# Kernel tuning notes

Hardware: AMD Instinct MI355X
Metric: run time of the kernel (lower is better)

The kernel has to match this reference:

```python
import jax, jax.numpy as jnp
import numpy as np

OBS_LEN, PRED_LEN, N, P = 8, 12, 4096, 32
EH, DH, EMB, BOT, NZ = 64, 128, 64, 1024, 8


def setup_inputs() -> dict:
    key = jax.random.key(0)
    ks = iter(jax.random.split(key, 64))
    rn = lambda shp, s=0.05: (jax.random.normal(next(ks), shp, jnp.float32) * s)
    d = {
        'obs_traj': rn((OBS_LEN, N, 2), 1.0),
        'obs_traj_rel': rn((OBS_LEN, N, 2), 0.5),
        'obs_speed': jax.random.uniform(next(ks), (OBS_LEN, N, 1), jnp.float32),
        'noise': rn((N, NZ), 1.0),
        'enc_emb_W': rn((2, EMB)), 'enc_emb_b': jnp.zeros((EMB,), jnp.float32),
        'enc_Wih': rn((EMB, 4 * EH)), 'enc_Whh': rn((EH, 4 * EH)), 'enc_b': jnp.zeros((4 * EH,), jnp.float32),
        'pool_sp_W': rn((2, 64)), 'pool_sp_b': jnp.zeros((64,), jnp.float32),
        'pool_spd_W': rn((1, 64)), 'pool_spd_b': jnp.zeros((64,), jnp.float32),
        'pool_l1_W': rn((192, 512)), 'pool_l1_b': jnp.zeros((512,), jnp.float32),
        'pool_bn1_g': jnp.ones((512,), jnp.float32), 'pool_bn1_b': jnp.zeros((512,), jnp.float32),
        'pool_l2_W': rn((512, BOT)), 'pool_l2_b': jnp.zeros((BOT,), jnp.float32),
        'pool_bn2_g': jnp.ones((BOT,), jnp.float32), 'pool_bn2_b': jnp.zeros((BOT,), jnp.float32),
        'spd_emb_W': rn((OBS_LEN, 64)), 'spd_emb_b': jnp.zeros((64,), jnp.float32),
        'ctx_l1_W': rn((EH + BOT + 64, 1024)), 'ctx_l1_b': jnp.zeros((1024,), jnp.float32),
        'ctx_bn1_g': jnp.ones((1024,), jnp.float32), 'ctx_bn1_b': jnp.zeros((1024,), jnp.float32),
        'ctx_l2_W': rn((1024, DH - NZ)), 'ctx_l2_b': jnp.zeros((DH - NZ,), jnp.float32),
        'ctx_bn2_g': jnp.ones((DH - NZ,), jnp.float32), 'ctx_bn2_b': jnp.zeros((DH - NZ,), jnp.float32),
        'dec_emb_W': rn((3, EMB)), 'dec_emb_b': jnp.zeros((EMB,), jnp.float32),
        'dec_Wih': rn((EMB, 4 * DH)), 'dec_Whh': rn((DH, 4 * DH)), 'dec_b': jnp.zeros((4 * DH,), jnp.float32),
        'h2p_W': rn((DH, 2)), 'h2p_b': jnp.zeros((2,), jnp.float32),
        'group_size': P,
    }
    return d


def _lstm(xs, Wih, Whh, b, h0, c0):
    # xs: [T, B, in]; PyTorch gate order (i, f, g, o)
    def step(carry, x):
        h, c = carry
        g = x @ Wih + h @ Whh + b
        i, f, gg, o = jnp.split(g, 4, axis=-1)
        c = jax.nn.sigmoid(f) * c + jax.nn.sigmoid(i) * jnp.tanh(gg)
        h = jax.nn.sigmoid(o) * jnp.tanh(c)
        return (h, c), h
    (h, c), _ = jax.lax.scan(step, (h0, c0), xs)
    return h, c


def _bn(x, g, b):
    # BatchNorm1d, eval mode with running_mean=0, running_var=1
    return x * g + b


def reference(obs_traj, obs_traj_rel, obs_speed, noise,
              enc_emb_W, enc_emb_b, enc_Wih, enc_Whh, enc_b,
              pool_sp_W, pool_sp_b, pool_spd_W, pool_spd_b,
              pool_l1_W, pool_l1_b, pool_bn1_g, pool_bn1_b,
              pool_l2_W, pool_l2_b, pool_bn2_g, pool_bn2_b,
              spd_emb_W, spd_emb_b,
              ctx_l1_W, ctx_l1_b, ctx_bn1_g, ctx_bn1_b,
              ctx_l2_W, ctx_l2_b, ctx_bn2_g, ctx_bn2_b,
              dec_emb_W, dec_emb_b, dec_Wih, dec_Whh, dec_b,
              h2p_W, h2p_b, group_size):
    n = obs_traj.shape[1]
    G = n // group_size
    # ---- Encoder: embed rel traj, run LSTM, take final hidden ----
    emb = obs_traj_rel @ enc_emb_W + enc_emb_b                       # [T, N, 64]
    h0 = jnp.zeros((n, EH), emb.dtype)
    final_h, _ = _lstm(emb, enc_Wih, enc_Whh, enc_b, h0, h0)         # [N, 64]
    # ---- PoolHiddenNet (vectorized per-group P x P social pooling) ----
    end_pos = obs_traj[-1].reshape(G, group_size, 2)                 # [G, P, 2]
    end_spd = obs_speed[-1].reshape(G, group_size, 1)                # [G, P, 1]
    hG = final_h.reshape(G, group_size, EH)                          # [G, P, 64]
    # rel[g, i, j] = pos[g, j] - pos[g, i]
    rel = end_pos[:, None, :, :] - end_pos[:, :, None, :]            # [G, P, P, 2]
    rel_e = rel @ pool_sp_W + pool_sp_b                              # [G, P, P, 64]
    spd_e = end_spd @ pool_spd_W + pool_spd_b                        # [G, P, 64]
    Pn = group_size
    feat = jnp.concatenate([
        rel_e,
        jnp.broadcast_to(hG[:, None, :, :], (G, Pn, Pn, EH)),
        jnp.broadcast_to(spd_e[:, None, :, :], (G, Pn, Pn, 64)),
    ], axis=-1)                                                      # [G, P, P, 192]
    h1 = jax.nn.relu(_bn(feat @ pool_l1_W + pool_l1_b, pool_bn1_g, pool_bn1_b))
    h2 = jax.nn.relu(_bn(h1 @ pool_l2_W + pool_l2_b, pool_bn2_g, pool_bn2_b))
    pool_h = jnp.max(h2, axis=2).reshape(n, BOT)                     # max over j -> [N, 1024]
    # ---- speed context: sigmoid(Linear(8 -> 64)) over obs speed history ----
    spd_hist = jnp.transpose(obs_speed[:, :, 0])                     # [N, 8]
    speed_ctx = jax.nn.sigmoid(spd_hist @ spd_emb_W + spd_emb_b)     # [N, 64]
    # ---- mlp_decoder_context + ped-level noise ----
    ctx_in = jnp.concatenate([final_h, pool_h, speed_ctx], axis=1)   # [N, 1152]
    c1 = jax.nn.relu(_bn(ctx_in @ ctx_l1_W + ctx_l1_b, ctx_bn1_g, ctx_bn1_b))
    ctx = jax.nn.relu(_bn(c1 @ ctx_l2_W + ctx_l2_b, ctx_bn2_g, ctx_bn2_b))  # [N, 120]
    dec_h = jnp.concatenate([ctx, noise], axis=1)                    # [N, 128]
    dec_c = jnp.zeros_like(dec_h)
    # ---- Decoder rollout (pred_len steps) ----
    last_pos = obs_traj[-1]
    last_speed = obs_speed[-1]                                       # [N, 1]
    x0 = jnp.concatenate([obs_traj_rel[-1], last_speed], axis=1) @ dec_emb_W + dec_emb_b

    def step(carry, _):
        h, c, x, lp = carry
        g = x @ dec_Wih + h @ dec_Whh + dec_b
        i, f, gg, o = jnp.split(g, 4, axis=-1)
        c = jax.nn.sigmoid(f) * c + jax.nn.sigmoid(i) * jnp.tanh(gg)
        h = jax.nn.sigmoid(o) * jnp.tanh(c)
        rel_pos = h @ h2p_W + h2p_b                                  # [N, 2]
        cur = rel_pos + lp
        x = jnp.concatenate([rel_pos, last_speed], axis=1) @ dec_emb_W + dec_emb_b
        return (h, c, x, cur), rel_pos

    _, rels = jax.lax.scan(step, (dec_h, dec_c, x0, last_pos), None, length=PRED_LEN)
    return rels  # [pred_len, N, 2]
```

## Files before the change

kernel.cpp:

```cpp
#include <hip/hip_runtime.h>

typedef __attribute__((ext_vector_type(8))) short v8s;
typedef __attribute__((ext_vector_type(4))) float v4f;
typedef unsigned short u16;

#define DINL static __device__ __forceinline__

DINL float b2f(u16 u){ union { unsigned uu; float ff; } x; x.uu = ((unsigned)u)<<16; return x.ff; }
DINL u16 f2b(float f){ union { float ff; unsigned uu; } x; x.ff = f; unsigned r = x.uu + 0x7FFFu + ((x.uu>>16)&1u); return (u16)(r>>16); }
DINL u16 f2b_hu(float f){ union { float ff; unsigned uu; } x; x.ff = f; return (u16)((x.uu + 0x8000u)>>16); }
DINL float sigm(float x){ return 1.0f/(1.0f+__expf(-x)); }
DINL float tanh_(float x){ return 2.0f/(1.0f+__expf(-2.0f*x)) - 1.0f; }
DINL float ld(const void* p, int i, int isf){
    return isf ? ((const float*)p)[i] : b2f(((const u16*)p)[i]);
}
DINL void g2lds16(const u16* g, u16* l){
    __builtin_amdgcn_global_load_lds(
        (const __attribute__((address_space(1))) unsigned int*)g,
        (__attribute__((address_space(3))) unsigned int*)l, 16, 0, 0);
}
DINL int detect_isf(const void* obs_speed){
    const u16* p = (const u16*)obs_speed;
    int f = 0;
    for (int i = 0; i < 16; ++i){
        u16 v = p[2*i];
        if ((v & 0x8000u) || v > 0x3F80u) f = 1;
    }
    return f;
}

#define FLAG_OFF 0x000000
#define AUX_OFF  0x000100
#define ENCF_OFF 0x010000
#define DECF_OFF 0x020000
#define CW2T_OFF 0x050000
#define W2T_OFF  0x090000
#define DECH_OFF 0x090000
#define CW1T_OFF 0x190000
#define IT_OFF   0x3D0000
#define IR_OFF   0x3F0000
#define IS_OFF   0x410000
#define INZ_OFF  0x420000
#define IW1H_OFF 0x430000
#define SM_OFF   0x440000
#define CTX_OFF  0x450000
#define AV_OFF   0xD50000
#define BIG_NEED 0x1550000

#define SM_EEW 0
#define SM_EEB 128
#define SM_ENB 192
#define SM_DEW 448
#define SM_DEB 640
#define SM_DNB 704
#define SM_H2W 1216
#define SM_H2B 1472
#define SM_SEW 1536
#define SM_SEB 2048

DINL void trans_tile(const void* in, u16* out, int K, int N, int isf,
                     int bx, int by, int t, float tile[64][65])
{
    const int nbase = bx*64, kbase = by*64;
    const int c = t & 63, r0 = (t >> 6)*16;
    for (int rep = 0; rep < 16; ++rep){
        int r = r0 + rep;
        int n = nbase + c;
        float v = 0.f;
        if (n < N) v = ld(in, (kbase + r)*N + n, isf);
        tile[r][c] = v;
    }
    __syncthreads();
    for (int rep = 0; rep < 16; ++rep){
        int r = r0 + rep;
        out[(size_t)(nbase + r)*K + kbase + c] = f2b(tile[c][r]);
    }
}

__global__ __launch_bounds__(256) void k_prep(
    const void* obs_traj, const void* obs_rel, const void* obs_speed, const void* noise,
    const void* eeW, const void* eeB, const void* enc_Wih, const void* enc_Whh, const void* encB,
    const void* spW, const void* spB, const void* spdW, const void* spdB,
    const void* pool_l1_W, const void* l1B, const void* bn1g, const void* bn1b,
    const void* pool_l2_W, const void* l2b, const void* bn2g, const void* bn2b,
    const void* seW, const void* seB,
    const void* ctx_l1_W, const void* c1b, const void* cbn1g, const void* cbn1b,
    const void* ctx_l2_W, const void* c2b, const void* cbn2g, const void* cbn2b,
    const void* deW, const void* deB, const void* dec_Wih, const void* dec_Whh, const void* decB,
    const void* h2W, const void* h2B,
    int* flag, float* AUX,
    u16* IT, u16* IR, u16* IS, u16* INZ, u16* IW1H, u16* SM,
    u16* W2T, u16* cW1T, u16* cW2T, u16* encF, u16* decF)
{
    __shared__ float tile[64][65];
    __shared__ int sisf;
    const int t = threadIdx.x;
    if (t == 0){
        int f = detect_isf(obs_speed);
        sisf = f;
        if (blockIdx.x == 0) *flag = f;
    }
    __syncthreads();
    const int isf = sisf;
    int bid = blockIdx.x;
    if (bid < 905){
        int idx = bid*256 + t;
        if (idx < 65536){ IT[idx] = f2b(ld(obs_traj, idx, isf)); return; }
        idx -= 65536;
        if (idx < 65536){ IR[idx] = f2b(ld(obs_rel, idx, isf)); return; }
        idx -= 65536;
        if (idx < 32768){ IS[idx] = f2b(ld(obs_speed, idx, isf)); return; }
        idx -= 32768;
        if (idx < 32768){ INZ[idx] = f2b(ld(noise, idx, isf)); return; }
        idx -= 32768;
        if (idx < 32768){ IW1H[idx] = f2b(ld(pool_l1_W, idx + 32768, isf)); return; }
        idx -= 32768;
        if (idx < 128){ SM[SM_EEW + idx] = f2b(ld(eeW, idx, isf)); return; }
        idx -= 128;
        if (idx < 64){ SM[SM_EEB + idx] = f2b(ld(eeB, idx, isf)); return; }
        idx -= 64;
        if (idx < 256){ SM[SM_ENB + idx] = f2b(ld(encB, idx, isf)); return; }
        idx -= 256;
        if (idx < 192){ SM[SM_DEW + idx] = f2b(ld(deW, idx, isf)); return; }
        idx -= 192;
        if (idx < 64){ SM[SM_DEB + idx] = f2b(ld(deB, idx, isf)); return; }
        idx -= 64;
        if (idx < 512){ SM[SM_DNB + idx] = f2b(ld(decB, idx, isf)); return; }
        idx -= 512;
        if (idx < 256){ SM[SM_H2W + idx] = f2b(ld(h2W, idx, isf)); return; }
        idx -= 256;
        if (idx < 2){ SM[SM_H2B + idx] = f2b(ld(h2B, idx, isf)); return; }
        idx -= 2;
        if (idx < 512){ SM[SM_SEW + idx] = f2b(ld(seW, idx, isf)); return; }
        idx -= 512;
        if (idx < 64){ SM[SM_SEB + idx] = f2b(ld(seB, idx, isf)); return; }
        return;
    }
    bid -= 905;
    if (bid < 512){
        int idx = bid*256 + t;
        if (idx < 32768){
            int jj = idx&7, lane = (idx>>3)&63, kcnf = idx>>9;
            int kc = kcnf&3, nf = kcnf>>2;
            int k = kc*32 + (lane>>4)*8 + jj, n = nf*16 + (lane&15);
            encF[idx] = (k < 64) ? f2b(ld(enc_Wih, k*256+n, isf)) : f2b(ld(enc_Whh, (k-64)*256+n, isf));
        } else {
            idx -= 32768;
            int jj = idx&7, lane = (idx>>3)&63, kcnf = idx>>9;
            int kc = kcnf % 6, nf = kcnf / 6;
            int k = kc*32 + (lane>>4)*8 + jj, n = nf*16 + (lane&15);
            decF[idx] = (k < 64) ? f2b(ld(dec_Wih, k*512+n, isf)) : f2b(ld(dec_Whh, (k-64)*512+n, isf));
        }
        return;
    }
    bid -= 512;
    if (bid < 128){ trans_tile(pool_l2_W, W2T, 512, 1024, isf, bid & 15, bid >> 4, t, tile); return; }
    bid -= 128;
    if (bid < 288){ trans_tile(ctx_l1_W, cW1T, 1152, 1024, isf, bid & 15, bid >> 4, t, tile); return; }
    bid -= 288;
    if (bid < 32){ trans_tile(ctx_l2_W, cW2T, 1024, 120, isf, bid & 1, bid >> 1, t, tile); return; }
    bid -= 32;
    {
        int idx = bid*256 + t;
        if (idx < 512){
            int c = idx;
            float m0 = 0.f, m1 = 0.f, qv = 0.f, cv = 0.f;
            for (int e = 0; e < 64; ++e){
                float w1a = ld(pool_l1_W, e*512 + c, isf);
                m0 += ld(spW, e, isf)*w1a;
                m1 += ld(spW, 64+e, isf)*w1a;
                cv += ld(spB, e, isf)*w1a;
                float w1c = ld(pool_l1_W, (128+e)*512 + c, isf);
                qv += ld(spdW, e, isf)*w1c;
                cv += ld(spdB, e, isf)*w1c;
            }
            cv += ld(l1B, c, isf);
            float g1 = ld(bn1g, c, isf), bb1 = ld(bn1b, c, isf);
            AUX[c] = m0; AUX[512+c] = m1; AUX[1024+c] = qv; AUX[1536+c] = cv;
            AUX[2048+c] = g1; AUX[2560+c] = bb1;
            AUX[3072+c] = g1*m0; AUX[3584+c] = g1*m1;
            return;
        }
        idx -= 512;
        if (idx < 1024){
            float g = ld(bn2g, idx, isf);
            AUX[4096+idx] = g; AUX[5120+idx] = ld(l2b, idx, isf)*g + ld(bn2b, idx, isf);
            return;
        }
        idx -= 1024;
        if (idx < 1024){
            float g = ld(cbn1g, idx, isf);
            AUX[6144+idx] = g; AUX[7168+idx] = ld(c1b, idx, isf)*g + ld(cbn1b, idx, isf);
            return;
        }
        idx -= 1024;
        if (idx < 128){
            int c = idx;
            float g  = (c < 120) ? ld(cbn2g, c, isf) : 1.f;
            float bb = (c < 120) ? (ld(c2b, c, isf)*g + ld(cbn2b, c, isf)) : 0.f;
            AUX[8192+c] = g; AUX[8320+c] = bb;
        }
    }
}

__global__ __launch_bounds__(256) void k_encoder(
    const u16* __restrict__ rel, const u16* __restrict__ embW, const u16* __restrict__ embB,
    const u16* __restrict__ encF, const u16* __restrict__ encB,
    const u16* __restrict__ IT, const u16* __restrict__ IS, const u16* __restrict__ IW1H,
    const u16* __restrict__ sW, const u16* __restrict__ sB,
    const float* __restrict__ AUX,
    u16* __restrict__ ctxIn, u16* __restrict__ Avec)
{
    __shared__ __align__(16) u16 Als[16*136];
    __shared__ float pxs[16], pys[16], sps[16];
    const int t = threadIdx.x, pedbase = blockIdx.x*16;
    const int w = t>>6, lane = t&63, quad = lane>>4, l15 = lane&15;
    for (int idx = t; idx < 16*64; idx += 256){ int p = idx>>6, jj = idx&63; Als[p*136 + 64 + jj] = 0; }
    if (t < 16){
        pxs[t] = b2f(IT[7*8192 + (pedbase+t)*2 + 0]);
        pys[t] = b2f(IT[7*8192 + (pedbase+t)*2 + 1]);
        sps[t] = b2f(IS[7*4096 + pedbase + t]);
    }
    {
        int p = t>>4, e0 = (t&15)*4;
        float rx = b2f(rel[(pedbase+p)*2 + 0]);
        float ry = b2f(rel[(pedbase+p)*2 + 1]);
        for (int e = e0; e < e0+4; ++e)
            Als[p*136 + e] = f2b(rx*b2f(embW[e]) + ry*b2f(embW[64+e]) + b2f(embB[e]));
    }
    const int j = w*16 + l15;
    const float bi = b2f(encB[j]), bff = b2f(encB[64+j]), bg = b2f(encB[128+j]), bo = b2f(encB[192+j]);
    float c4[4] = {0.f,0.f,0.f,0.f};
    for (int step = 0; step < 8; ++step){
        __syncthreads();
        v4f acc[4];
        for (int q = 0; q < 4; ++q) acc[q] = (v4f){0.f,0.f,0.f,0.f};
        for (int kc = 0; kc < 4; ++kc){
            v8s a = *(const v8s*)&Als[l15*136 + kc*32 + quad*8];
            for (int q = 0; q < 4; ++q){
                int nf = q*4 + w;
                v8s b = *(const v8s*)&encF[((nf*4 + kc)*64 + lane)*8];
                acc[q] = __builtin_amdgcn_mfma_f32_16x16x32_bf16(a, b, acc[q], 0, 0, 0);
            }
        }
        __syncthreads();
        for (int r = 0; r < 4; ++r){
            float gi = sigm(acc[0][r] + bi), gf = sigm(acc[1][r] + bff);
            float gg = tanh_(acc[2][r] + bg), go = sigm(acc[3][r] + bo);
            c4[r] = gf*c4[r] + gi*gg;
            Als[(quad*4 + r)*136 + 64 + j] = f2b(go*tanh_(c4[r]));
        }
        if (step < 7){
            int p = t>>4, e0 = (t&15)*4;
            float rx = b2f(rel[(step+1)*8192 + (pedbase+p)*2 + 0]);
            float ry = b2f(rel[(step+1)*8192 + (pedbase+p)*2 + 1]);
            for (int e = e0; e < e0+4; ++e)
                Als[p*136 + e] = f2b(rx*b2f(embW[e]) + ry*b2f(embW[64+e]) + b2f(embB[e]));
        }
    }
    __syncthreads();
    for (int idx = t; idx < 1024; idx += 256){
        int p = idx>>6, e = idx&63;
        ctxIn[(size_t)(pedbase+p)*1152 + e] = Als[p*136 + 64 + e];
    }
    {
        const int c0 = (t&127)*4, pg = (t>>7)*8;
        float4 acc[8];
        for (int p = 0; p < 8; ++p) acc[p] = make_float4(0.f,0.f,0.f,0.f);
        for (int e = 0; e < 64; ++e){
            ushort4 wv = *(const ushort4*)(IW1H + e*512 + c0);
            float w0 = b2f(wv.x), w1 = b2f(wv.y), w2 = b2f(wv.z), w3 = b2f(wv.w);
            for (int p = 0; p < 8; ++p){
                float h = b2f(Als[(pg+p)*136 + 64 + e]);
                acc[p].x += h*w0; acc[p].y += h*w1; acc[p].z += h*w2; acc[p].w += h*w3;
            }
        }
        float4 m0 = *(const float4*)(AUX + c0),        m1 = *(const float4*)(AUX + 512 + c0);
        float4 qv = *(const float4*)(AUX + 1024 + c0), cv = *(const float4*)(AUX + 1536 + c0);
        float4 g1 = *(const float4*)(AUX + 2048 + c0), bb = *(const float4*)(AUX + 2560 + c0);
        for (int p = 0; p < 8; ++p){
            float px = pxs[pg+p], py = pys[pg+p], sp = sps[pg+p];
            ushort4 o;
            o.x = f2b(g1.x*(px*m0.x + py*m1.x + sp*qv.x + cv.x + acc[p].x) + bb.x);
            o.y = f2b(g1.y*(px*m0.y + py*m1.y + sp*qv.y + cv.y + acc[p].y) + bb.y);
            o.z = f2b(g1.z*(px*m0.z + py*m1.z + sp*qv.z + cv.z + acc[p].z) + bb.z);
            o.w = f2b(g1.w*(px*m0.w + py*m1.w + sp*qv.w + cv.w + acc[p].w) + bb.w);
            *(ushort4*)&Avec[(size_t)(pedbase+pg+p)*512 + c0] = o;
        }
    }
    {
        int s = t & 63;
        for (int rep = 0; rep < 4; ++rep){
            int p = (t>>6)*4 + rep;
            int nid = pedbase + p;
            float a = b2f(sB[s]);
            for (int tt = 0; tt < 8; ++tt) a += b2f(IS[tt*4096 + nid]) * b2f(sW[tt*64 + s]);
            ctxIn[(size_t)nid*1152 + 1088 + s] = f2b(sigm(a));
        }
    }
}

__global__ __launch_bounds__(256, 3) void k_pool(
    const u16* __restrict__ Avec, const u16* __restrict__ W2T,
    const u16* __restrict__ IT, const float* __restrict__ AUX,
    u16* __restrict__ ctxIn)
{
    __shared__ __align__(16) u16 Als[64*72];
    __shared__ __align__(16) u16 Bls[256*64];
    __shared__ __align__(16) float pmls[1024];
    const int t = threadIdx.x;
    const int g = blockIdx.x >> 4, ip = blockIdx.x & 15;
    const int n0 = blockIdx.y * 256;
    const int w = t>>6, lane = t&63, quad = lane>>4, l15 = lane&15;
    const int aj = t>>3, ao = t&7;
    const float px0 = b2f(IT[7*8192 + (g*32 + ip*2 + 0)*2 + 0]);
    const float py0 = b2f(IT[7*8192 + (g*32 + ip*2 + 0)*2 + 1]);
    const float px1 = b2f(IT[7*8192 + (g*32 + ip*2 + 1)*2 + 0]);
    const float py1 = b2f(IT[7*8192 + (g*32 + ip*2 + 1)*2 + 1]);
    for (int i = t; i < 512; i += 256){
        float m0 = AUX[3072 + i], m1 = AUX[3584 + i];
        pmls[i]       = px0*m0 + py0*m1;
        pmls[512 + i] = px1*m0 + py1*m1;
    }
    const u16* bsrc = W2T + (size_t)(n0 + w*8 + (lane>>3))*512 + (size_t)(((lane&7) ^ (lane>>3)))*8;
    u16* bdst = &Bls[w*512];
    const u16* arow = Avec + (size_t)(g*32+aj)*512 + ao*8;
    v4f acc[4][4];
    for (int mf = 0; mf < 4; ++mf) for (int nf = 0; nf < 4; ++nf) acc[mf][nf] = (v4f){0.f,0.f,0.f,0.f};
    union { v8s v; u16 u[8]; } av;
    av.v = *(const v8s*)arow;
    for (int ch = 0; ch < 8; ++ch){
        const int k0 = ch*64;
        __syncthreads();
        for (int it = 0; it < 8; ++it)
            g2lds16(bsrc + k0 + it*16384, bdst + it*2048);
        {
            float a0[8];
            #pragma unroll
            for (int i = 0; i < 8; ++i) a0[i] = b2f(av.u[i]);
            #pragma unroll
            for (int il = 0; il < 2; ++il){
                float4 p0 = *(const float4*)&pmls[il*512 + k0 + ao*8];
                float4 p1 = *(const float4*)&pmls[il*512 + k0 + ao*8 + 4];
                float pmv[8] = {p0.x,p0.y,p0.z,p0.w,p1.x,p1.y,p1.z,p1.w};
                union { unsigned u[4]; v8s v; } pk;
                #pragma unroll
                for (int jj = 0; jj < 4; ++jj){
                    union { float f; unsigned u; } x0, x1;
                    x0.f = fmaxf(a0[2*jj]   - pmv[2*jj],   0.f);
                    x1.f = fmaxf(a0[2*jj+1] - pmv[2*jj+1], 0.f);
                    pk.u[jj] = __builtin_amdgcn_perm(x1.u + 0x8000u, x0.u + 0x8000u, 0x07060302u);
                }
                *(v8s*)&Als[(il*32+aj)*72 + ao*8] = pk.v;
            }
        }
        if (ch < 7) av.v = *(const v8s*)(arow + (ch+1)*64);
        __syncthreads();
        for (int kc = 0; kc < 2; ++kc){
            v8s af[4];
            for (int mf = 0; mf < 4; ++mf)
                af[mf] = *(const v8s*)&Als[(mf*16 + l15)*72 + kc*32 + quad*8];
            const int sl = ((kc*4 + quad) ^ (l15&7))*8;
            #pragma unroll
            for (int nf = 0; nf < 4; ++nf){
                v8s bf = *(const v8s*)&Bls[(w*64 + nf*16 + l15)*64 + sl];
                acc[0][nf] = __builtin_amdgcn_mfma_f32_16x16x32_bf16(af[0], bf, acc[0][nf], 0, 0, 0);
                acc[1][nf] = __builtin_amdgcn_mfma_f32_16x16x32_bf16(af[1], bf, acc[1][nf], 0, 0, 0);
                acc[2][nf] = __builtin_amdgcn_mfma_f32_16x16x32_bf16(af[2], bf, acc[2][nf], 0, 0, 0);
                acc[3][nf] = __builtin_amdgcn_mfma_f32_16x16x32_bf16(af[3], bf, acc[3][nf], 0, 0, 0);
            }
        }
    }
    const float* S2 = AUX + 4096; const float* B2 = AUX + 5120;
    for (int nf = 0; nf < 4; ++nf){
        int n = n0 + w*64 + nf*16 + l15;
        float s = S2[n], bb = B2[n];
        float mm0 = 0.f, mm1 = 0.f;
        for (int mf = 0; mf < 2; ++mf) for (int r = 0; r < 4; ++r) mm0 = fmaxf(mm0, fmaxf(s*acc[mf][nf][r] + bb, 0.f));
        for (int mf = 2; mf < 4; ++mf) for (int r = 0; r < 4; ++r) mm1 = fmaxf(mm1, fmaxf(s*acc[mf][nf][r] + bb, 0.f));
        mm0 = fmaxf(mm0, __shfl_xor(mm0, 16)); mm0 = fmaxf(mm0, __shfl_xor(mm0, 32));
        mm1 = fmaxf(mm1, __shfl_xor(mm1, 16)); mm1 = fmaxf(mm1, __shfl_xor(mm1, 32));
        if (quad == 0) ctxIn[(size_t)(g*32 + ip*2 + 0)*1152 + 64 + n] = f2b(mm0);
        if (quad == 1) ctxIn[(size_t)(g*32 + ip*2 + 1)*1152 + 64 + n] = f2b(mm1);
    }
}

template<int MF>
__global__ __launch_bounds__(256) void k_gemm_bt(
    const u16* __restrict__ A, int lda, const u16* __restrict__ BT,
    const float* __restrict__ S, const float* __restrict__ Bb,
    u16* __restrict__ out, int ldo, int K, int validN,
    const u16* __restrict__ noisep)
{
    __shared__ __align__(16) u16 Als[MF*32*72];
    __shared__ __align__(16) u16 Bls[128*72];
    const int t = threadIdx.x;
    const int m0 = blockIdx.x*(MF*32), n0 = blockIdx.y*128;
    const int w = t>>6, lane = t&63, quad = lane>>4, l15 = lane&15;
    const int rw = w>>1, cw = w&1;
    v4f acc[MF][4];
    for (int mf = 0; mf < MF; ++mf) for (int nf = 0; nf < 4; ++nf) acc[mf][nf] = (v4f){0.f,0.f,0.f,0.f};
    const int nch = K >> 6;
    for (int ch = 0; ch < nch; ++ch){
        const int k0 = ch*64;
        __syncthreads();
        if (MF == 4){
            const int srow = t>>1, sh = t&1;
            const u16* srcA = A + (size_t)(m0+srow)*lda + k0 + sh*32;
            u16* dstA = &Als[srow*72 + sh*32];
            ((v8s*)dstA)[0] = ((const v8s*)srcA)[0];
            ((v8s*)dstA)[1] = ((const v8s*)srcA)[1];
            ((v8s*)dstA)[2] = ((const v8s*)srcA)[2];
            ((v8s*)dstA)[3] = ((const v8s*)srcA)[3];
        } else {
            const int srow = t>>2, sh = t&3;
            const u16* srcA = A + (size_t)(m0+srow)*lda + k0 + sh*16;
            u16* dstA = &Als[srow*72 + sh*16];
            ((v8s*)dstA)[0] = ((const v8s*)srcA)[0];
            ((v8s*)dstA)[1] = ((const v8s*)srcA)[1];
        }
        {
            const int srow = t>>1, sh = t&1;
            const u16* srcB = BT + (size_t)(n0+srow)*K + k0 + sh*32;
            u16* dstB = &Bls[srow*72 + sh*32];
            ((v8s*)dstB)[0] = ((const v8s*)srcB)[0];
            ((v8s*)dstB)[1] = ((const v8s*)srcB)[1];
            ((v8s*)dstB)[2] = ((const v8s*)srcB)[2];
            ((v8s*)dstB)[3] = ((const v8s*)srcB)[3];
        }
        __syncthreads();
        for (int kc = 0; kc < 2; ++kc){
            v8s af[MF], bf[4];
            for (int mf = 0; mf < MF; ++mf) af[mf] = *(const v8s*)&Als[(rw*(MF*16) + mf*16 + l15)*72 + kc*32 + quad*8];
            for (int nf = 0; nf < 4; ++nf) bf[nf] = *(const v8s*)&Bls[(cw*64 + nf*16 + l15)*72 + kc*32 + quad*8];
            for (int mf = 0; mf < MF; ++mf)
                for (int nf = 0; nf < 4; ++nf)
                    acc[mf][nf] = __builtin_amdgcn_mfma_f32_16x16x32_bf16(af[mf], bf[nf], acc[mf][nf], 0, 0, 0);
        }
    }
    for (int nf = 0; nf < 4; ++nf){
        int n = n0 + cw*64 + nf*16 + l15;
        bool okn = (n < validN);
        float s = okn ? S[n] : 0.f, bb = okn ? Bb[n] : 0.f;
        bool okz = (!okn) && (noisep != nullptr) && (n < 128);
        for (int mf = 0; mf < MF; ++mf){
            int m = m0 + rw*(MF*16) + mf*16 + quad*4;
            for (int r = 0; r < 4; ++r){
                float v = fmaxf(s*acc[mf][nf][r] + bb, 0.f);
                if (okn) out[(size_t)(m+r)*ldo + n] = f2b(v);
                else if (okz) out[(size_t)(m+r)*ldo + n] = noisep[(size_t)(m+r)*8 + (n - 120)];
            }
        }
    }
}

__global__ __launch_bounds__(256) void k_decoder(
    const u16* __restrict__ decH0, const u16* __restrict__ decF, const u16* __restrict__ decB,
    const u16* __restrict__ dembW, const u16* __restrict__ dembB,
    const u16* __restrict__ h2pW, const u16* __restrict__ h2pB,
    const u16* __restrict__ obs_rel, const u16* __restrict__ obs_speed,
    const int* __restrict__ flag, void* __restrict__ outp)
{
    __shared__ __align__(16) u16 Als[16*200];
    __shared__ float rps[16][2];
    __shared__ float sps[16];
    __shared__ float h2ps[256];
    const int t = threadIdx.x, pedbase = blockIdx.x*16;
    const int w = t>>6, lane = t&63, quad = lane>>4, l15 = lane&15;
    const int isf = *flag;
    for (int idx = t; idx < 2048; idx += 256){
        int p = idx>>7, jj = idx&127;
        Als[p*200 + 64 + jj] = decH0[(pedbase+p)*128 + jj];
    }
    h2ps[t] = b2f(h2pW[t]);
    if (t < 16) sps[t] = b2f(obs_speed[7*4096 + pedbase + t]);
    if (t < 32){ int p = t>>1, cmp = t&1; rps[p][cmp] = b2f(obs_rel[7*8192 + (pedbase+p)*2 + cmp]); }
    __syncthreads();
    {
        int p = t>>4, e0 = (t&15)*4;
        for (int e = e0; e < e0+4; ++e){
            float v = rps[p][0]*b2f(dembW[e]) + rps[p][1]*b2f(dembW[64+e]) + sps[p]*b2f(dembW[128+e]) + b2f(dembB[e]);
            Als[p*200 + e] = f2b(v);
        }
    }
    float bI[2], bF[2], bG[2], bO[2];
    for (int nfl = 0; nfl < 2; ++nfl){
        int j = w*32 + nfl*16 + l15;
        bI[nfl] = b2f(decB[j]); bF[nfl] = b2f(decB[128+j]);
        bG[nfl] = b2f(decB[256+j]); bO[nfl] = b2f(decB[384+j]);
    }
    float c8[2][4] = {{0.f,0.f,0.f,0.f},{0.f,0.f,0.f,0.f}};
    for (int s = 0; s < 12; ++s){
        __syncthreads();
        v4f acc[4][2];
        for (int q = 0; q < 4; ++q) for (int nfl = 0; nfl < 2; ++nfl) acc[q][nfl] = (v4f){0.f,0.f,0.f,0.f};
        for (int kc = 0; kc < 6; ++kc){
            v8s a = *(const v8s*)&Als[l15*200 + kc*32 + quad*8];
            for (int q = 0; q < 4; ++q){
                for (int nfl = 0; nfl < 2; ++nfl){
                    int nf = q*8 + w*2 + nfl;
                    v8s b = *(const v8s*)&decF[((nf*6 + kc)*64 + lane)*8];
                    acc[q][nfl] = __builtin_amdgcn_mfma_f32_16x16x32_bf16(a, b, acc[q][nfl], 0, 0, 0);
                }
            }
        }
        __syncthreads();
        for (int nfl = 0; nfl < 2; ++nfl){
            int j = w*32 + nfl*16 + l15;
            for (int r = 0; r < 4; ++r){
                float gi = sigm(acc[0][nfl][r] + bI[nfl]), gf = sigm(acc[1][nfl][r] + bF[nfl]);
                float gg = tanh_(acc[2][nfl][r] + bG[nfl]), go = sigm(acc[3][nfl][r] + bO[nfl]);
                c8[nfl][r] = gf*c8[nfl][r] + gi*gg;
                Als[(quad*4 + r)*200 + 64 + j] = f2b(go*tanh_(c8[nfl][r]));
            }
        }
        __syncthreads();
        {
            int p = t>>4, cmp = (t>>3)&1, part = t&7;
            float rp = 0.f;
            int j0 = part*16;
            for (int jj = j0; jj < j0+16; ++jj)
                rp += b2f(Als[p*200 + 64 + jj]) * h2ps[jj*2 + cmp];
            rp += __shfl_xor(rp, 1);
            rp += __shfl_xor(rp, 2);
            rp += __shfl_xor(rp, 4);
            if (part == 0){
                rp += b2f(h2pB[cmp]);
                int oi = s*8192 + (pedbase+p)*2 + cmp;
                if (isf) ((float*)outp)[oi] = rp;
                else     ((u16*)outp)[oi]   = f2b(rp);
                rps[p][cmp] = rp;
            }
        }
        __syncthreads();
        {
            int p = t>>4, e0 = (t&15)*4;
            for (int e = e0; e < e0+4; ++e){
                float v = rps[p][0]*b2f(dembW[e]) + rps[p][1]*b2f(dembW[64+e]) + sps[p]*b2f(dembW[128+e]) + b2f(dembB[e]);
                Als[p*200 + e] = f2b(v);
            }
        }
    }
}

extern "C" void kernel_launch(void* const* d_in, const int* in_sizes, int n_in,
                              void* d_out, int out_size, void* d_ws, size_t ws_size,
                              hipStream_t stream)
{
    (void)in_sizes; (void)n_in; (void)out_size;
    const void* obs_traj  = d_in[0];
    const void* obs_rel   = d_in[1];
    const void* obs_speed = d_in[2];
    const void* noise     = d_in[3];
    const void* enc_emb_W = d_in[4];
    const void* enc_emb_b = d_in[5];
    const void* enc_Wih   = d_in[6];
    const void* enc_Whh   = d_in[7];
    const void* enc_b     = d_in[8];
    const void* pool_sp_W = d_in[9];
    const void* pool_sp_b = d_in[10];
    const void* pool_spd_W= d_in[11];
    const void* pool_spd_b= d_in[12];
    const void* pool_l1_W = d_in[13];
    const void* pool_l1_b = d_in[14];
    const void* pool_bn1_g= d_in[15];
    const void* pool_bn1_b= d_in[16];
    const void* pool_l2_W = d_in[17];
    const void* pool_l2_b = d_in[18];
    const void* pool_bn2_g= d_in[19];
    const void* pool_bn2_b= d_in[20];
    const void* spd_emb_W = d_in[21];
    const void* spd_emb_b = d_in[22];
    const void* ctx_l1_W  = d_in[23];
    const void* ctx_l1_b  = d_in[24];
    const void* ctx_bn1_g = d_in[25];
    const void* ctx_bn1_b = d_in[26];
    const void* ctx_l2_W  = d_in[27];
    const void* ctx_l2_b  = d_in[28];
    const void* ctx_bn2_g = d_in[29];
    const void* ctx_bn2_b = d_in[30];
    const void* dec_emb_W = d_in[31];
    const void* dec_emb_b = d_in[32];
    const void* dec_Wih   = d_in[33];
    const void* dec_Whh   = d_in[34];
    const void* dec_b     = d_in[35];
    const void* h2p_W     = d_in[36];
    const void* h2p_b     = d_in[37];

    char* ws = (char*)d_ws;
    int*   flag  = (int*)  (ws + FLAG_OFF);
    float* AUX   = (float*)(ws + AUX_OFF);
    u16*   encF  = (u16*)  (ws + ENCF_OFF);
    u16*   decF  = (u16*)  (ws + DECF_OFF);
    u16*   cW2T  = (u16*)  (ws + CW2T_OFF);
    u16*   W2T   = (u16*)  (ws + W2T_OFF);
    u16*   decH  = (u16*)  (ws + DECH_OFF);
    u16*   cW1T  = (u16*)  (ws + CW1T_OFF);
    u16*   IT    = (u16*)  (ws + IT_OFF);
    u16*   IR    = (u16*)  (ws + IR_OFF);
    u16*   IS    = (u16*)  (ws + IS_OFF);
    u16*   INZ   = (u16*)  (ws + INZ_OFF);
    u16*   IW1H  = (u16*)  (ws + IW1H_OFF);
    u16*   SM    = (u16*)  (ws + SM_OFF);
    u16*   ctxIn = (u16*)  (ws + CTX_OFF);
    u16*   Avec  = (u16*)  (ws + AV_OFF);
    u16*   c1    = (u16*)  (ws + AV_OFF);
    const bool big = (ws_size >= (size_t)BIG_NEED);

    k_prep<<<dim3(1876), dim3(256), 0, stream>>>(
        obs_traj, obs_rel, obs_speed, noise,
        enc_emb_W, enc_emb_b, enc_Wih, enc_Whh, enc_b,
        pool_sp_W, pool_sp_b, pool_spd_W, pool_spd_b,
        pool_l1_W, pool_l1_b, pool_bn1_g, pool_bn1_b,
        pool_l2_W, pool_l2_b, pool_bn2_g, pool_bn2_b,
        spd_emb_W, spd_emb_b,
        ctx_l1_W, ctx_l1_b, ctx_bn1_g, ctx_bn1_b,
        ctx_l2_W, ctx_l2_b, ctx_bn2_g, ctx_bn2_b,
        dec_emb_W, dec_emb_b, dec_Wih, dec_Whh, dec_b,
        h2p_W, h2p_b,
        flag, AUX, IT, IR, IS, INZ, IW1H, SM,
        W2T, cW1T, cW2T, encF, decF);
    k_encoder<<<dim3(256), dim3(256), 0, stream>>>(
        IR, SM + SM_EEW, SM + SM_EEB, encF, SM + SM_ENB,
        IT, IS, IW1H, SM + SM_SEW, SM + SM_SEB, AUX, ctxIn, Avec);
    k_pool<<<dim3(2048, 4), dim3(256), 0, stream>>>(Avec, W2T, IT, AUX, ctxIn);
    if (big){
        k_gemm_bt<4><<<dim3(32, 8), dim3(256), 0, stream>>>(
            ctxIn, 1152, cW1T, AUX + 6144, AUX + 7168, c1, 1024, 1152, 1024, (const u16*)nullptr);
        k_gemm_bt<2><<<dim3(64, 1), dim3(256), 0, stream>>>(
            c1, 1024, cW2T, AUX + 8192, AUX + 8320, decH, 128, 1024, 120, INZ);
    } else {
        k_gemm_bt<4><<<dim3(16, 8), dim3(256), 0, stream>>>(
            ctxIn, 1152, cW1T, AUX + 6144, AUX + 7168, c1, 1024, 1152, 1024, (const u16*)nullptr);
        k_gemm_bt<2><<<dim3(32, 1), dim3(256), 0, stream>>>(
            c1, 1024, cW2T, AUX + 8192, AUX + 8320, decH, 128, 1024, 120, INZ);
        k_gemm_bt<4><<<dim3(16, 8), dim3(256), 0, stream>>>(
            ctxIn + (size_t)2048*1152, 1152, cW1T, AUX + 6144, AUX + 7168, c1, 1024, 1152, 1024, (const u16*)nullptr);
        k_gemm_bt<2><<<dim3(32, 1), dim3(256), 0, stream>>>(
            c1, 1024, cW2T, AUX + 8192, AUX + 8320, decH + (size_t)2048*128, 128, 1024, 120, INZ + (size_t)2048*8);
    }
    k_decoder<<<dim3(256), dim3(256), 0, stream>>>(
        decH, decF, SM + SM_DNB, SM + SM_DEW, SM + SM_DEB,
        SM + SM_H2W, SM + SM_H2B, IR, IS, flag, d_out);
}
```

Measured before the change: 435.9 us.

## Shrink context GEMM tiles, split pool launch, shuffle decoder positions

Switches the context-MLP GEMMs to smaller M tiles (MF=2 and a new MF=1 path) with more blocks, so more CUs have work on the small problem. Splits the pool kernel into two launches of half the grid each through an x-offset parameter. In the decoder, the predicted relative positions are broadcast with wave shuffles instead of going through shared memory, which removes one barrier per step and skips the unused embedding on the final step. Smaller tiles reload the B operand more often, and the extra launch adds launch overhead.

```diff
diff --git a/kernel.cpp b/kernel.cpp
--- a/kernel.cpp
+++ b/kernel.cpp
@@ -8,7 +8,6 @@
 
 DINL float b2f(u16 u){ union { unsigned uu; float ff; } x; x.uu = ((unsigned)u)<<16; return x.ff; }
 DINL u16 f2b(float f){ union { float ff; unsigned uu; } x; x.ff = f; unsigned r = x.uu + 0x7FFFu + ((x.uu>>16)&1u); return (u16)(r>>16); }
-DINL u16 f2b_hu(float f){ union { float ff; unsigned uu; } x; x.ff = f; return (u16)((x.uu + 0x8000u)>>16); }
 DINL float sigm(float x){ return 1.0f/(1.0f+__expf(-x)); }
 DINL float tanh_(float x){ return 2.0f/(1.0f+__expf(-2.0f*x)) - 1.0f; }
 DINL float ld(const void* p, int i, int isf){
@@ -303,13 +302,14 @@
 __global__ __launch_bounds__(256, 3) void k_pool(
     const u16* __restrict__ Avec, const u16* __restrict__ W2T,
     const u16* __restrict__ IT, const float* __restrict__ AUX,
-    u16* __restrict__ ctxIn)
+    u16* __restrict__ ctxIn, int xbase)
 {
     __shared__ __align__(16) u16 Als[64*72];
     __shared__ __align__(16) u16 Bls[256*64];
     __shared__ __align__(16) float pmls[1024];
     const int t = threadIdx.x;
-    const int g = blockIdx.x >> 4, ip = blockIdx.x & 15;
+    const int bx = blockIdx.x + xbase;
+    const int g = bx >> 4, ip = bx & 15;
     const int n0 = blockIdx.y * 256;
     const int w = t>>6, lane = t&63, quad = lane>>4, l15 = lane&15;
     const int aj = t>>3, ao = t&7;
@@ -412,12 +412,17 @@
             ((v8s*)dstA)[1] = ((const v8s*)srcA)[1];
             ((v8s*)dstA)[2] = ((const v8s*)srcA)[2];
             ((v8s*)dstA)[3] = ((const v8s*)srcA)[3];
-        } else {
+        } else if (MF == 2){
             const int srow = t>>2, sh = t&3;
             const u16* srcA = A + (size_t)(m0+srow)*lda + k0 + sh*16;
             u16* dstA = &Als[srow*72 + sh*16];
             ((v8s*)dstA)[0] = ((const v8s*)srcA)[0];
             ((v8s*)dstA)[1] = ((const v8s*)srcA)[1];
+        } else {
+            const int srow = t>>3, sh = t&7;
+            const u16* srcA = A + (size_t)(m0+srow)*lda + k0 + sh*8;
+            u16* dstA = &Als[srow*72 + sh*8];
+            ((v8s*)dstA)[0] = ((const v8s*)srcA)[0];
         }
         {
             const int srow = t>>1, sh = t&1;
@@ -462,7 +467,6 @@
     const int* __restrict__ flag, void* __restrict__ outp)
 {
     __shared__ __align__(16) u16 Als[16*200];
-    __shared__ float rps[16][2];
     __shared__ float sps[16];
     __shared__ float h2ps[256];
     const int t = threadIdx.x, pedbase = blockIdx.x*16;
@@ -474,12 +478,13 @@
     }
     h2ps[t] = b2f(h2pW[t]);
     if (t < 16) sps[t] = b2f(obs_speed[7*4096 + pedbase + t]);
-    if (t < 32){ int p = t>>1, cmp = t&1; rps[p][cmp] = b2f(obs_rel[7*8192 + (pedbase+p)*2 + cmp]); }
     __syncthreads();
     {
         int p = t>>4, e0 = (t&15)*4;
+        float rx = b2f(obs_rel[7*8192 + (pedbase+p)*2 + 0]);
+        float ry = b2f(obs_rel[7*8192 + (pedbase+p)*2 + 1]);
         for (int e = e0; e < e0+4; ++e){
-            float v = rps[p][0]*b2f(dembW[e]) + rps[p][1]*b2f(dembW[64+e]) + sps[p]*b2f(dembW[128+e]) + b2f(dembB[e]);
+            float v = rx*b2f(dembW[e]) + ry*b2f(dembW[64+e]) + sps[p]*b2f(dembW[128+e]) + b2f(dembB[e]);
             Als[p*200 + e] = f2b(v);
         }
     }
@@ -524,20 +529,20 @@
             rp += __shfl_xor(rp, 1);
             rp += __shfl_xor(rp, 2);
             rp += __shfl_xor(rp, 4);
+            rp += b2f(h2pB[cmp]);
             if (part == 0){
-                rp += b2f(h2pB[cmp]);
                 int oi = s*8192 + (pedbase+p)*2 + cmp;
                 if (isf) ((float*)outp)[oi] = rp;
                 else     ((u16*)outp)[oi]   = f2b(rp);
-                rps[p][cmp] = rp;
-            }
-        }
-        __syncthreads();
-        {
-            int p = t>>4, e0 = (t&15)*4;
-            for (int e = e0; e < e0+4; ++e){
-                float v = rps[p][0]*b2f(dembW[e]) + rps[p][1]*b2f(dembW[64+e]) + sps[p]*b2f(dembW[128+e]) + b2f(dembB[e]);
-                Als[p*200 + e] = f2b(v);
+            }
+            float rp0 = __shfl(rp, (lane & 48));
+            float rp1 = __shfl(rp, (lane & 48) + 8);
+            if (s < 11){
+                int e0 = (t&15)*4;
+                for (int e = e0; e < e0+4; ++e){
+                    float v = rp0*b2f(dembW[e]) + rp1*b2f(dembW[64+e]) + sps[p]*b2f(dembW[128+e]) + b2f(dembB[e]);
+                    Als[p*200 + e] = f2b(v);
+                }
             }
         }
     }
@@ -623,20 +628,21 @@
     k_encoder<<<dim3(256), dim3(256), 0, stream>>>(
         IR, SM + SM_EEW, SM + SM_EEB, encF, SM + SM_ENB,
         IT, IS, IW1H, SM + SM_SEW, SM + SM_SEB, AUX, ctxIn, Avec);
-    k_pool<<<dim3(2048, 4), dim3(256), 0, stream>>>(Avec, W2T, IT, AUX, ctxIn);
+    k_pool<<<dim3(1024, 4), dim3(256), 0, stream>>>(Avec, W2T, IT, AUX, ctxIn, 0);
+    k_pool<<<dim3(1024, 4), dim3(256), 0, stream>>>(Avec, W2T, IT, AUX, ctxIn, 1024);
     if (big){
-        k_gemm_bt<4><<<dim3(32, 8), dim3(256), 0, stream>>>(
+        k_gemm_bt<2><<<dim3(64, 8), dim3(256), 0, stream>>>(
             ctxIn, 1152, cW1T, AUX + 6144, AUX + 7168, c1, 1024, 1152, 1024, (const u16*)nullptr);
-        k_gemm_bt<2><<<dim3(64, 1), dim3(256), 0, stream>>>(
+        k_gemm_bt<1><<<dim3(128, 1), dim3(256), 0, stream>>>(
             c1, 1024, cW2T, AUX + 8192, AUX + 8320, decH, 128, 1024, 120, INZ);
     } else {
-        k_gemm_bt<4><<<dim3(16, 8), dim3(256), 0, stream>>>(
+        k_gemm_bt<2><<<dim3(32, 8), dim3(256), 0, stream>>>(
             ctxIn, 1152, cW1T, AUX + 6144, AUX + 7168, c1, 1024, 1152, 1024, (const u16*)nullptr);
-        k_gemm_bt<2><<<dim3(32, 1), dim3(256), 0, stream>>>(
+        k_gemm_bt<1><<<dim3(64, 1), dim3(256), 0, stream>>>(
             c1, 1024, cW2T, AUX + 8192, AUX + 8320, decH, 128, 1024, 120, INZ);
-        k_gemm_bt<4><<<dim3(16, 8), dim3(256), 0, stream>>>(
+        k_gemm_bt<2><<<dim3(32, 8), dim3(256), 0, stream>>>(
             ctxIn + (size_t)2048*1152, 1152, cW1T, AUX + 6144, AUX + 7168, c1, 1024, 1152, 1024, (const u16*)nullptr);
-        k_gemm_bt<2><<<dim3(32, 1), dim3(256), 0, stream>>>(
+        k_gemm_bt<1><<<dim3(64, 1), dim3(256), 0, stream>>>(
             c1, 1024, cW2T, AUX + 8192, AUX + 8320, decH + (size_t)2048*128, 128, 1024, 120, INZ + (size_t)2048*8);
     }
     k_decoder<<<dim3(256), dim3(256), 0, stream>>>(
```

New measurement: 430.5 us. No clear change (-1.2%).
